# Performance work log

Hardware: AMD Instinct MI355X
Metric: run time of the kernel (lower is better)

## Reference

```python
import jax, jax.numpy as jnp
import numpy as np

N_NODES = 100000
N_EDGES = 1600000
F_IN = 128
N_HEADS = 4
F_OUT = 32
NEG_SLOPE = 0.2


def setup_inputs() -> dict:
    key = jax.random.key(0)
    k_feat, k_src, k_dst, k_w, k_as, k_ad, k_res = jax.random.split(key, 7)
    feat = jax.random.normal(k_feat, (N_NODES, F_IN), dtype=jnp.float32)
    src = jax.random.randint(k_src, (N_EDGES,), 0, N_NODES, dtype=jnp.int32)
    dst = jax.random.randint(k_dst, (N_EDGES,), 0, N_NODES, dtype=jnp.int32)
    s = 1.0 / np.sqrt(F_IN)
    W = jax.random.normal(k_w, (F_IN, N_HEADS * F_OUT), dtype=jnp.float32) * s
    att_src = jax.random.normal(k_as, (N_HEADS, F_OUT), dtype=jnp.float32) * 0.1
    att_dst = jax.random.normal(k_ad, (N_HEADS, F_OUT), dtype=jnp.float32) * 0.1
    W_res = jax.random.normal(k_res, (F_IN, N_HEADS * F_OUT), dtype=jnp.float32) * s
    return {"feat": feat, "W": W, "att_src": att_src, "att_dst": att_dst,
            "W_res": W_res, "src": src, "dst": dst}


def reference(feat, W, att_src, att_dst, W_res, src, dst):
    N = feat.shape[0]
    H, Fo = att_src.shape
    # shared linear projection (GATConv, bias=False): [N, H, Fo]
    x = (feat @ W).reshape(N, H, Fo)
    # per-node attention logits: [N, H]
    a_s = jnp.einsum('nhf,hf->nh', x, att_src)
    a_d = jnp.einsum('nhf,hf->nh', x, att_dst)
    # edge-wise scores + LeakyReLU: [E, H]
    e = jax.nn.leaky_relu(a_s[src] + a_d[dst], negative_slope=NEG_SLOPE)
    # segment softmax over incoming edges of each dst node
    e_max = jax.ops.segment_max(e, dst, num_segments=N)  # [N, H]
    e_exp = jnp.exp(e - e_max[dst])                       # [E, H]
    denom = jax.ops.segment_sum(e_exp, dst, num_segments=N)  # [N, H]
    alpha = e_exp / denom[dst]                            # [E, H]
    # weighted scatter-add aggregation: [N, H, Fo]
    msg = x[src] * alpha[:, :, None]
    out = jax.ops.segment_sum(msg, dst, num_segments=N)
    # residual projection
    res = (feat @ W_res).reshape(N, H, Fo)
    return out + res
```

## Files before the change

kernel.cpp:

```cpp
#include <hip/hip_runtime.h>
#include <math.h>

#define NN 100000
#define NE 1600000
#define F_IN 128
#define C 128
#define NEG_SLOPE 0.2f
#define PROJ_NB ((NN + 63) / 64)

#define NBLK1 256
#define EPB ((NE + NBLK1 - 1) / NBLK1)
#define BSHIFT 9
#define NBUCK ((NN + 511) / 512)

typedef __attribute__((ext_vector_type(8))) short short8;
typedef __attribute__((ext_vector_type(4))) float f32x4;
typedef __attribute__((ext_vector_type(4))) float floatx4;
typedef __attribute__((ext_vector_type(4))) unsigned short ushortx4;

static __device__ __forceinline__ unsigned short f2bf(float f) {
    unsigned int u = __float_as_uint(f);
    unsigned int r = (u + 0x7fff + ((u >> 16) & 1)) >> 16;
    return (unsigned short)r;
}
static __device__ __forceinline__ float bf2f(unsigned short h) {
    return __uint_as_float((unsigned int)h << 16);
}

__global__ __launch_bounds__(256)
void wconv_kernel(const float* __restrict__ W,
                  const float* __restrict__ Wr,
                  unsigned short* __restrict__ Btf)
{
    int g = blockIdx.x * 256 + threadIdx.x;
    int nt = g >> 8;
    int kc = (g >> 6) & 3;
    int l  = g & 63;
    int n  = nt * 16 + (l & 15);
    int kb = kc * 32 + (l >> 4) * 8;
    unsigned short v[8];
    #pragma unroll
    for (int j = 0; j < 8; ++j) {
        int k = kb + j;
        float f = (n < 128) ? W[(size_t)k * 128 + n] : Wr[(size_t)k * 128 + (n - 128)];
        v[j] = f2bf(f);
    }
    *(short8*)&Btf[(size_t)g * 8] = *(short8*)v;
}

__global__ __launch_bounds__(256, 4)
void proj_kernel(const float* __restrict__ feat,
                 const unsigned short* __restrict__ Btf,
                 const float* __restrict__ att_src,
                 const float* __restrict__ att_dst,
                 unsigned short* __restrict__ xb,
                 unsigned short* __restrict__ resb,
                 float* __restrict__ a_s,
                 float* __restrict__ a_d)
{
    __shared__ __align__(16) float T2all[4][16 * 68];
    __shared__ float s_as[64][4];
    __shared__ float s_ad[64][4];
    const int tid = threadIdx.x;

    const int base = blockIdx.x * 64;
    const int l = tid & 63;
    const int w = tid >> 6;
    const int quad = l >> 4;
    const int lo16 = l & 15;
    const int arow = w * 16 + lo16;
    const int nclamp = min(base + arow, NN - 1);

    short8 af[4];
    #pragma unroll
    for (int kc = 0; kc < 4; ++kc) {
        const float* fp = &feat[(size_t)nclamp * F_IN + kc * 32 + quad * 8];
        floatx4 f0 = __builtin_nontemporal_load((const floatx4*)fp);
        floatx4 f1 = __builtin_nontemporal_load((const floatx4*)(fp + 4));
        unsigned short v[8];
        v[0] = f2bf(f0.x); v[1] = f2bf(f0.y); v[2] = f2bf(f0.z); v[3] = f2bf(f0.w);
        v[4] = f2bf(f1.x); v[5] = f2bf(f1.y); v[6] = f2bf(f1.z); v[7] = f2bf(f1.w);
        af[kc] = *(short8*)v;
    }

    f32x4 acc[16];
    #pragma unroll
    for (int nt = 0; nt < 16; ++nt) acc[nt] = (f32x4){0.f, 0.f, 0.f, 0.f};

    #pragma unroll
    for (int nt = 0; nt < 16; ++nt) {
        const unsigned short* bp = &Btf[(size_t)(nt * 4) * 512 + l * 8];
        short8 b0 = *(const short8*)&bp[0];
        short8 b1 = *(const short8*)&bp[512];
        short8 b2 = *(const short8*)&bp[1024];
        short8 b3 = *(const short8*)&bp[1536];
        acc[nt] = __builtin_amdgcn_mfma_f32_16x16x32_bf16(af[0], b0, acc[nt], 0, 0, 0);
        acc[nt] = __builtin_amdgcn_mfma_f32_16x16x32_bf16(af[1], b1, acc[nt], 0, 0, 0);
        acc[nt] = __builtin_amdgcn_mfma_f32_16x16x32_bf16(af[2], b2, acc[nt], 0, 0, 0);
        acc[nt] = __builtin_amdgcn_mfma_f32_16x16x32_bf16(af[3], b3, acc[nt], 0, 0, 0);
    }

    float* T2 = T2all[w];
    const int g  = l >> 4;
    const int cf = (l & 15) * 4;

    #pragma unroll
    for (int p = 0; p < 2; ++p) {
        #pragma unroll
        for (int ntl = 0; ntl < 4; ++ntl) {
            int nt = p * 4 + ntl;
            #pragma unroll
            for (int r = 0; r < 4; ++r)
                T2[(quad * 4 + r) * 68 + ntl * 16 + lo16] = acc[nt][r];
        }
        floatx4 ws4 = *(const floatx4*)&att_src[p * 64 + cf];
        floatx4 wd4 = *(const floatx4*)&att_dst[p * 64 + cf];
        float ps[4], pd[4];
        #pragma unroll
        for (int it = 0; it < 4; ++it) {
            int row = it * 4 + g;
            floatx4 v = *(floatx4*)&T2[row * 68 + cf];
            int node = base + w * 16 + row;
            ushortx4 hh;
            hh.x = f2bf(v.x); hh.y = f2bf(v.y); hh.z = f2bf(v.z); hh.w = f2bf(v.w);
            if (node < NN)
                __builtin_nontemporal_store(hh,
                    (ushortx4*)&xb[(size_t)node * C + p * 64 + cf]);
            ps[it] = v.x * ws4.x + v.y * ws4.y + v.z * ws4.z + v.w * ws4.w;
            pd[it] = v.x * wd4.x + v.y * wd4.y + v.z * wd4.z + v.w * wd4.w;
        }
        #pragma unroll
        for (int it = 0; it < 4; ++it) {
            #pragma unroll
            for (int d = 1; d < 8; d <<= 1) {
                ps[it] += __shfl_xor(ps[it], d, 64);
                pd[it] += __shfl_xor(pd[it], d, 64);
            }
        }
        if ((l & 7) == 0) {
            int hh = p * 2 + ((l & 15) >> 3);
            #pragma unroll
            for (int it = 0; it < 4; ++it) {
                int lr = w * 16 + it * 4 + g;
                s_as[lr][hh] = ps[it];
                s_ad[lr][hh] = pd[it];
            }
        }
    }

    #pragma unroll
    for (int p = 0; p < 2; ++p) {
        #pragma unroll
        for (int ntl = 0; ntl < 4; ++ntl) {
            int nt = 8 + p * 4 + ntl;
            #pragma unroll
            for (int r = 0; r < 4; ++r)
                T2[(quad * 4 + r) * 68 + ntl * 16 + lo16] = acc[nt][r];
        }
        #pragma unroll
        for (int it = 0; it < 4; ++it) {
            int row = it * 4 + g;
            floatx4 v = *(floatx4*)&T2[row * 68 + cf];
            int node = base + w * 16 + row;
            ushortx4 hh;
            hh.x = f2bf(v.x); hh.y = f2bf(v.y); hh.z = f2bf(v.z); hh.w = f2bf(v.w);
            if (node < NN)
                __builtin_nontemporal_store(hh,
                    (ushortx4*)&resb[(size_t)node * C + p * 64 + cf]);
        }
    }

    __syncthreads();
    int idx = blockIdx.x * 256 + tid;
    if (idx < NN * 4) {
        a_s[idx] = ((float*)s_as)[tid];
        a_d[idx] = ((float*)s_ad)[tid];
    }
}

__global__ __launch_bounds__(256)
void sort1_kernel(const int* __restrict__ dst, int* __restrict__ counts)
{
    __shared__ int h[256];
    const int tid = threadIdx.x;
    h[tid] = 0;
    __syncthreads();
    const int e0 = blockIdx.x * EPB;
    const int e1 = min(NE, e0 + EPB);
    for (int e = e0 + tid; e < e1; e += 256)
        atomicAdd(&h[dst[e] >> BSHIFT], 1);
    __syncthreads();
    counts[blockIdx.x * 256 + tid] = h[tid];
}

__global__ __launch_bounds__(256)
void sortscan_kernel(int* __restrict__ counts, int* __restrict__ bucket_base)
{
    __shared__ int wsum[4];
    const int t = threadIdx.x, lane = t & 63, wid = t >> 6;
    int run = 0;
    #pragma unroll 8
    for (int b = 0; b < NBLK1; ++b) {
        int v = counts[b * 256 + t];
        counts[b * 256 + t] = run;
        run += v;
    }
    int v0 = run, v = run;
    #pragma unroll
    for (int off = 1; off < 64; off <<= 1) {
        int u = __shfl_up(v, off, 64);
        if (lane >= off) v += u;
    }
    if (lane == 63) wsum[wid] = v;
    __syncthreads();
    if (t == 0) {
        int r = 0;
        #pragma unroll
        for (int s = 0; s < 4; ++s) { int tmp = wsum[s]; wsum[s] = r; r += tmp; }
    }
    __syncthreads();
    int excl = wsum[wid] + (v - v0);
    bucket_base[t] = excl;
    if (t == 255) bucket_base[256] = excl + v0;
}

__global__ __launch_bounds__(256)
void sort2_kernel(const int* __restrict__ src, const int* __restrict__ dst,
                  const int* __restrict__ counts,
                  const int* __restrict__ bucket_base,
                  int* __restrict__ bpack)
{
    __shared__ int cur[256];
    const int tid = threadIdx.x;
    cur[tid] = bucket_base[tid] + counts[blockIdx.x * 256 + tid];
    __syncthreads();
    const int e0 = blockIdx.x * EPB;
    const int e1 = min(NE, e0 + EPB);
    for (int e = e0 + tid; e < e1; e += 256) {
        int d = dst[e];
        int s = src[e];
        int pos = atomicAdd(&cur[d >> BSHIFT], 1);
        bpack[pos] = ((d & 511) << 20) | s;
    }
}

__global__ __launch_bounds__(512)
void sort3_kernel(const int* __restrict__ bpack,
                  const int* __restrict__ bucket_base,
                  int* __restrict__ row_ptr,
                  int* __restrict__ csr_src)
{
    __shared__ int cnt[512];
    __shared__ int cur[512];
    __shared__ int wsum[8];
    const int t = threadIdx.x, lane = t & 63, wid = t >> 6;
    const int b = blockIdx.x;
    const int ebeg = bucket_base[b];
    const int eend = bucket_base[b + 1];
    cnt[t] = 0;
    __syncthreads();
    for (int e = ebeg + t; e < eend; e += 512)
        atomicAdd(&cnt[bpack[e] >> 20], 1);
    __syncthreads();
    int v0 = cnt[t], v = v0;
    #pragma unroll
    for (int off = 1; off < 64; off <<= 1) {
        int u = __shfl_up(v, off, 64);
        if (lane >= off) v += u;
    }
    if (lane == 63) wsum[wid] = v;
    __syncthreads();
    if (t == 0) {
        int r = 0;
        #pragma unroll
        for (int s = 0; s < 8; ++s) { int tmp = wsum[s]; wsum[s] = r; r += tmp; }
    }
    __syncthreads();
    int excl = wsum[wid] + (v - v0);
    cur[t] = excl;
    int n = (b << BSHIFT) + t;
    if (n < NN) row_ptr[n] = ebeg + excl;
    if (b == NBUCK - 1 && t == 0) row_ptr[NN] = NE;
    __syncthreads();
    for (int e = ebeg + t; e < eend; e += 512) {
        int p = bpack[e];
        int pos = atomicAdd(&cur[p >> 20], 1);
        csr_src[ebeg + pos] = p & 0xFFFFF;
    }
}

__global__ __launch_bounds__(256)
void agg_kernel(const unsigned short* __restrict__ xb,
                const unsigned short* __restrict__ resb,
                const float* __restrict__ a_s,
                const float* __restrict__ a_d,
                const int* __restrict__ row_ptr,
                const int* __restrict__ csr_src,
                float* __restrict__ out)
{
    __shared__ float s_alpha[4][4][68];
    __shared__ int   s_srcs[4][4][17];
    const int tid = threadIdx.x;
    const int w   = tid >> 6;
    const int l   = tid & 63;
    const int q   = l >> 4;
    const int t16 = l & 15;
    const int h   = t16 >> 2;

    const int n = blockIdx.x * 16 + w * 4 + q;
    const int r0  = row_ptr[n];
    const int deg = row_ptr[n + 1] - r0;

    short8 rv = *(const short8*)&resb[(size_t)n * C + t16 * 8];
    const float4 ad4 = *(const float4*)&a_d[n * 4];

    int dm = deg;
    dm = max(dm, __shfl_xor(dm, 16, 64));
    dm = max(dm, __shfl_xor(dm, 32, 64));

    float acc8[8];
    #pragma unroll
    for (int j = 0; j < 8; ++j) acc8[j] = 0.f;
    float dx = 0.f, dy = 0.f, dz = 0.f, dw = 0.f;

    for (int c0 = 0; c0 < dm; c0 += 16) {
        int e = c0 + t16;
        int s = 0;
        float4 ex = {0.f, 0.f, 0.f, 0.f};
        if (e < deg) {
            s = csr_src[r0 + e];
            float4 as4 = *(const float4*)&a_s[s * 4];
            float e0 = as4.x + ad4.x, e1 = as4.y + ad4.y;
            float e2 = as4.z + ad4.z, e3 = as4.w + ad4.w;
            e0 = (e0 > 0.f) ? e0 : NEG_SLOPE * e0;
            e1 = (e1 > 0.f) ? e1 : NEG_SLOPE * e1;
            e2 = (e2 > 0.f) ? e2 : NEG_SLOPE * e2;
            e3 = (e3 > 0.f) ? e3 : NEG_SLOPE * e3;
            ex.x = __expf(e0); ex.y = __expf(e1);
            ex.z = __expf(e2); ex.w = __expf(e3);
            dx += ex.x; dy += ex.y; dz += ex.z; dw += ex.w;
        }
        s_srcs[w][q][t16] = s;
        *(float4*)&s_alpha[w][q][t16 * 4] = ex;

        int cn = min(16, deg - c0);
        #pragma unroll 2
        for (int i = 0; i < cn; ++i) {
            int   si = s_srcs[w][q][i];
            float al = s_alpha[w][q][i * 4 + h];
            short8 uv = *(const short8*)&xb[(size_t)si * C + t16 * 8];
            acc8[0] = fmaf(al, bf2f((unsigned short)uv[0]), acc8[0]);
            acc8[1] = fmaf(al, bf2f((unsigned short)uv[1]), acc8[1]);
            acc8[2] = fmaf(al, bf2f((unsigned short)uv[2]), acc8[2]);
            acc8[3] = fmaf(al, bf2f((unsigned short)uv[3]), acc8[3]);
            acc8[4] = fmaf(al, bf2f((unsigned short)uv[4]), acc8[4]);
            acc8[5] = fmaf(al, bf2f((unsigned short)uv[5]), acc8[5]);
            acc8[6] = fmaf(al, bf2f((unsigned short)uv[6]), acc8[6]);
            acc8[7] = fmaf(al, bf2f((unsigned short)uv[7]), acc8[7]);
        }
    }

    #pragma unroll
    for (int d = 1; d < 16; d <<= 1) {
        dx += __shfl_xor(dx, d, 64);
        dy += __shfl_xor(dy, d, 64);
        dz += __shfl_xor(dz, d, 64);
        dw += __shfl_xor(dw, d, 64);
    }
    float den = (h == 0) ? dx : (h == 1) ? dy : (h == 2) ? dz : dw;
    float inv = (deg > 0) ? 1.f / den : 0.f;

    floatx4 o0, o1;
    o0.x = bf2f((unsigned short)rv[0]) + acc8[0] * inv;
    o0.y = bf2f((unsigned short)rv[1]) + acc8[1] * inv;
    o0.z = bf2f((unsigned short)rv[2]) + acc8[2] * inv;
    o0.w = bf2f((unsigned short)rv[3]) + acc8[3] * inv;
    o1.x = bf2f((unsigned short)rv[4]) + acc8[4] * inv;
    o1.y = bf2f((unsigned short)rv[5]) + acc8[5] * inv;
    o1.z = bf2f((unsigned short)rv[6]) + acc8[6] * inv;
    o1.w = bf2f((unsigned short)rv[7]) + acc8[7] * inv;
    __builtin_nontemporal_store(o0, (floatx4*)&out[(size_t)n * C + t16 * 8]);
    __builtin_nontemporal_store(o1, (floatx4*)&out[(size_t)n * C + t16 * 8 + 4]);
}

extern "C" void kernel_launch(void* const* d_in, const int* in_sizes, int n_in,
                              void* d_out, int out_size, void* d_ws, size_t ws_size,
                              hipStream_t stream)
{
    const float* feat    = (const float*)d_in[0];
    const float* W       = (const float*)d_in[1];
    const float* att_src = (const float*)d_in[2];
    const float* att_dst = (const float*)d_in[3];
    const float* W_res   = (const float*)d_in[4];
    const int*   src     = (const int*)d_in[5];
    const int*   dst     = (const int*)d_in[6];
    float* out = (float*)d_out;

    char* p = (char*)d_ws;
    unsigned short* xb   = (unsigned short*)p; p += (size_t)NN * C * sizeof(unsigned short);
    unsigned short* resb = (unsigned short*)p; p += (size_t)NN * C * sizeof(unsigned short);
    unsigned short* Btf  = (unsigned short*)p; p += (size_t)256 * 128 * sizeof(unsigned short);
    float* a_s = (float*)p;            p += (size_t)NN * 4 * sizeof(float);
    float* a_d = (float*)p;            p += (size_t)NN * 4 * sizeof(float);
    int* row_ptr = (int*)p;            p += (size_t)(NN + 1) * sizeof(int);
    int* counts  = (int*)p;            p += (size_t)NBLK1 * 256 * sizeof(int);
    int* bucket_base = (int*)p;        p += (size_t)257 * sizeof(int);
    int* bpack   = (int*)p;            p += (size_t)NE * sizeof(int);
    int* csr_src = (int*)p;            p += (size_t)NE * sizeof(int);

    wconv_kernel<<<16, 256, 0, stream>>>(W, W_res, Btf);
    proj_kernel<<<PROJ_NB, 256, 0, stream>>>(
        feat, Btf, att_src, att_dst, xb, resb, a_s, a_d);
    sort1_kernel<<<NBLK1, 256, 0, stream>>>(dst, counts);
    sortscan_kernel<<<1, 256, 0, stream>>>(counts, bucket_base);
    sort2_kernel<<<NBLK1, 256, 0, stream>>>(src, dst, counts, bucket_base, bpack);
    sort3_kernel<<<NBUCK, 512, 0, stream>>>(bpack, bucket_base, row_ptr, csr_src);
    agg_kernel<<<NN / 16, 256, 0, stream>>>(xb, resb, a_s, a_d, row_ptr, csr_src, out);
}
```

Measured before the change: 264.9 us.

## Edge-balanced aggregation with precomputed softmax denominators in sort pass

The softmax denominators are now computed in the bucket-sort kernel with LDS atomics and stored as inverse values, and the CSR keeps the packed local-dst bits. The aggregation kernel changes from one 16-lane group per node to 64 nodes per block, with each group taking an equal slice of the block's edges. Partial sums go into LDS accumulators through atomics whenever the destination changes, and the source gathers are software-pipelined two edges ahead. This targets load imbalance from varying degrees, at the cost of extra exp work and a_s/a_d gathers in sort3 plus LDS atomic traffic.

```diff
diff --git a/kernel.cpp b/kernel.cpp
--- a/kernel.cpp
+++ b/kernel.cpp
@@ -13,6 +13,10 @@
 #define BSHIFT 9
 #define NBUCK ((NN + 511) / 512)
 
+#define AGG_NB 64
+#define AGG_GRID ((NN + AGG_NB - 1) / AGG_NB)
+#define ASTRIDE 132
+
 typedef __attribute__((ext_vector_type(8))) short short8;
 typedef __attribute__((ext_vector_type(4))) float f32x4;
 typedef __attribute__((ext_vector_type(4))) float floatx4;
@@ -25,6 +29,9 @@
 }
 static __device__ __forceinline__ float bf2f(unsigned short h) {
     return __uint_as_float((unsigned int)h << 16);
+}
+static __device__ __forceinline__ float lrelu(float x) {
+    return (x > 0.f) ? x : NEG_SLOPE * x;
 }
 
 __global__ __launch_bounds__(256)
@@ -247,20 +254,36 @@
 __global__ __launch_bounds__(512)
 void sort3_kernel(const int* __restrict__ bpack,
                   const int* __restrict__ bucket_base,
+                  const float* __restrict__ a_s,
+                  const float* __restrict__ a_d,
                   int* __restrict__ row_ptr,
-                  int* __restrict__ csr_src)
+                  int* __restrict__ csr_pack,
+                  float* __restrict__ inv_den)
 {
     __shared__ int cnt[512];
-    __shared__ int cur[512];
+    __shared__ int curs[512];
     __shared__ int wsum[8];
+    __shared__ float sden[512 * 4];
     const int t = threadIdx.x, lane = t & 63, wid = t >> 6;
     const int b = blockIdx.x;
     const int ebeg = bucket_base[b];
     const int eend = bucket_base[b + 1];
     cnt[t] = 0;
-    __syncthreads();
-    for (int e = ebeg + t; e < eend; e += 512)
-        atomicAdd(&cnt[bpack[e] >> 20], 1);
+    #pragma unroll
+    for (int j = 0; j < 4; ++j) sden[t + j * 512] = 0.f;
+    __syncthreads();
+    for (int e = ebeg + t; e < eend; e += 512) {
+        int p = bpack[e];
+        int dl = p >> 20;
+        int s  = p & 0xFFFFF;
+        atomicAdd(&cnt[dl], 1);
+        float4 as4 = *(const float4*)&a_s[(size_t)s * 4];
+        float4 ad4 = *(const float4*)&a_d[(size_t)((b << BSHIFT) + dl) * 4];
+        atomicAdd(&sden[dl * 4 + 0], __expf(lrelu(as4.x + ad4.x)));
+        atomicAdd(&sden[dl * 4 + 1], __expf(lrelu(as4.y + ad4.y)));
+        atomicAdd(&sden[dl * 4 + 2], __expf(lrelu(as4.z + ad4.z)));
+        atomicAdd(&sden[dl * 4 + 3], __expf(lrelu(as4.w + ad4.w)));
+    }
     __syncthreads();
     int v0 = cnt[t], v = v0;
     #pragma unroll
@@ -277,15 +300,23 @@
     }
     __syncthreads();
     int excl = wsum[wid] + (v - v0);
-    cur[t] = excl;
+    curs[t] = excl;
     int n = (b << BSHIFT) + t;
-    if (n < NN) row_ptr[n] = ebeg + excl;
+    if (n < NN) {
+        row_ptr[n] = ebeg + excl;
+        float d0 = sden[t * 4 + 0], d1 = sden[t * 4 + 1];
+        float d2 = sden[t * 4 + 2], d3 = sden[t * 4 + 3];
+        inv_den[n * 4 + 0] = (d0 > 0.f) ? 1.f / d0 : 0.f;
+        inv_den[n * 4 + 1] = (d1 > 0.f) ? 1.f / d1 : 0.f;
+        inv_den[n * 4 + 2] = (d2 > 0.f) ? 1.f / d2 : 0.f;
+        inv_den[n * 4 + 3] = (d3 > 0.f) ? 1.f / d3 : 0.f;
+    }
     if (b == NBUCK - 1 && t == 0) row_ptr[NN] = NE;
     __syncthreads();
     for (int e = ebeg + t; e < eend; e += 512) {
         int p = bpack[e];
-        int pos = atomicAdd(&cur[p >> 20], 1);
-        csr_src[ebeg + pos] = p & 0xFFFFF;
+        int pos = atomicAdd(&curs[p >> 20], 1);
+        csr_pack[ebeg + pos] = p;
     }
 }
 
@@ -294,93 +325,122 @@
                 const unsigned short* __restrict__ resb,
                 const float* __restrict__ a_s,
                 const float* __restrict__ a_d,
+                const float* __restrict__ inv_den,
                 const int* __restrict__ row_ptr,
-                const int* __restrict__ csr_src,
+                const int* __restrict__ csr_pack,
                 float* __restrict__ out)
 {
-    __shared__ float s_alpha[4][4][68];
-    __shared__ int   s_srcs[4][4][17];
+    __shared__ float accL[AGG_NB * ASTRIDE];
+    __shared__ float lds_ad[AGG_NB * 4];
+    __shared__ float lds_inv[AGG_NB * 4];
     const int tid = threadIdx.x;
-    const int w   = tid >> 6;
-    const int l   = tid & 63;
-    const int q   = l >> 4;
-    const int t16 = l & 15;
+    const int n0 = blockIdx.x * AGG_NB;
+
+    {
+        int nidx = n0 * 4 + tid;
+        float adv = 0.f, ivv = 0.f;
+        if (nidx < NN * 4) { adv = a_d[nidx]; ivv = inv_den[nidx]; }
+        lds_ad[tid] = adv;
+        lds_inv[tid] = ivv;
+    }
+    #pragma unroll
+    for (int i = 0; i < (AGG_NB * ASTRIDE) / 256; ++i)
+        accL[tid + i * 256] = 0.f;
+
+    const int rp0 = row_ptr[n0];
+    const int rpN = row_ptr[min(n0 + AGG_NB, NN)];
+    __syncthreads();
+
+    const int ecnt = rpN - rp0;
+    const int gq  = tid >> 4;
+    const int t16 = tid & 15;
     const int h   = t16 >> 2;
-
-    const int n = blockIdx.x * 16 + w * 4 + q;
-    const int r0  = row_ptr[n];
-    const int deg = row_ptr[n + 1] - r0;
-
-    short8 rv = *(const short8*)&resb[(size_t)n * C + t16 * 8];
-    const float4 ad4 = *(const float4*)&a_d[n * 4];
-
-    int dm = deg;
-    dm = max(dm, __shfl_xor(dm, 16, 64));
-    dm = max(dm, __shfl_xor(dm, 32, 64));
-
-    float acc8[8];
-    #pragma unroll
-    for (int j = 0; j < 8; ++j) acc8[j] = 0.f;
-    float dx = 0.f, dy = 0.f, dz = 0.f, dw = 0.f;
-
-    for (int c0 = 0; c0 < dm; c0 += 16) {
-        int e = c0 + t16;
-        int s = 0;
-        float4 ex = {0.f, 0.f, 0.f, 0.f};
-        if (e < deg) {
-            s = csr_src[r0 + e];
-            float4 as4 = *(const float4*)&a_s[s * 4];
-            float e0 = as4.x + ad4.x, e1 = as4.y + ad4.y;
-            float e2 = as4.z + ad4.z, e3 = as4.w + ad4.w;
-            e0 = (e0 > 0.f) ? e0 : NEG_SLOPE * e0;
-            e1 = (e1 > 0.f) ? e1 : NEG_SLOPE * e1;
-            e2 = (e2 > 0.f) ? e2 : NEG_SLOPE * e2;
-            e3 = (e3 > 0.f) ? e3 : NEG_SLOPE * e3;
-            ex.x = __expf(e0); ex.y = __expf(e1);
-            ex.z = __expf(e2); ex.w = __expf(e3);
-            dx += ex.x; dy += ex.y; dz += ex.z; dw += ex.w;
-        }
-        s_srcs[w][q][t16] = s;
-        *(float4*)&s_alpha[w][q][t16 * 4] = ex;
-
-        int cn = min(16, deg - c0);
-        #pragma unroll 2
-        for (int i = 0; i < cn; ++i) {
-            int   si = s_srcs[w][q][i];
-            float al = s_alpha[w][q][i * 4 + h];
-            short8 uv = *(const short8*)&xb[(size_t)si * C + t16 * 8];
-            acc8[0] = fmaf(al, bf2f((unsigned short)uv[0]), acc8[0]);
-            acc8[1] = fmaf(al, bf2f((unsigned short)uv[1]), acc8[1]);
-            acc8[2] = fmaf(al, bf2f((unsigned short)uv[2]), acc8[2]);
-            acc8[3] = fmaf(al, bf2f((unsigned short)uv[3]), acc8[3]);
-            acc8[4] = fmaf(al, bf2f((unsigned short)uv[4]), acc8[4]);
-            acc8[5] = fmaf(al, bf2f((unsigned short)uv[5]), acc8[5]);
-            acc8[6] = fmaf(al, bf2f((unsigned short)uv[6]), acc8[6]);
-            acc8[7] = fmaf(al, bf2f((unsigned short)uv[7]), acc8[7]);
-        }
-    }
-
-    #pragma unroll
-    for (int d = 1; d < 16; d <<= 1) {
-        dx += __shfl_xor(dx, d, 64);
-        dy += __shfl_xor(dy, d, 64);
-        dz += __shfl_xor(dz, d, 64);
-        dw += __shfl_xor(dw, d, 64);
-    }
-    float den = (h == 0) ? dx : (h == 1) ? dy : (h == 2) ? dz : dw;
-    float inv = (deg > 0) ? 1.f / den : 0.f;
-
-    floatx4 o0, o1;
-    o0.x = bf2f((unsigned short)rv[0]) + acc8[0] * inv;
-    o0.y = bf2f((unsigned short)rv[1]) + acc8[1] * inv;
-    o0.z = bf2f((unsigned short)rv[2]) + acc8[2] * inv;
-    o0.w = bf2f((unsigned short)rv[3]) + acc8[3] * inv;
-    o1.x = bf2f((unsigned short)rv[4]) + acc8[4] * inv;
-    o1.y = bf2f((unsigned short)rv[5]) + acc8[5] * inv;
-    o1.z = bf2f((unsigned short)rv[6]) + acc8[6] * inv;
-    o1.w = bf2f((unsigned short)rv[7]) + acc8[7] * inv;
-    __builtin_nontemporal_store(o0, (floatx4*)&out[(size_t)n * C + t16 * 8]);
-    __builtin_nontemporal_store(o1, (floatx4*)&out[(size_t)n * C + t16 * 8 + 4]);
+    const int chunk = (ecnt + 15) >> 4;
+    const int ebeg = rp0 + gq * chunk;
+    const int eend = min(rpN, ebeg + chunk);
+
+    if (ebeg < eend) {
+        int p0 = csr_pack[ebeg];
+        int s0 = p0 & 0xFFFFF;
+        float as0 = a_s[(size_t)s0 * 4 + h];
+        short8 uv0 = *(const short8*)&xb[(size_t)s0 * C + t16 * 8];
+        int p1 = p0; float as1 = as0; short8 uv1 = uv0;
+        if (ebeg + 1 < eend) {
+            p1 = csr_pack[ebeg + 1];
+            int s1 = p1 & 0xFFFFF;
+            as1 = a_s[(size_t)s1 * 4 + h];
+            uv1 = *(const short8*)&xb[(size_t)s1 * C + t16 * 8];
+        }
+
+        int cur = (p0 >> 20) & 63;
+        float ad_h  = lds_ad[cur * 4 + h];
+        float inv_h = lds_inv[cur * 4 + h];
+        float a0 = 0.f, a1 = 0.f, a2 = 0.f, a3 = 0.f;
+        float a4 = 0.f, a5 = 0.f, a6 = 0.f, a7 = 0.f;
+
+        for (int e = ebeg; e < eend; ++e) {
+            int p2 = p0; float as2 = as0; short8 uv2 = uv0;
+            if (e + 2 < eend) {
+                p2 = csr_pack[e + 2];
+                int s2 = p2 & 0xFFFFF;
+                as2 = a_s[(size_t)s2 * 4 + h];
+                uv2 = *(const short8*)&xb[(size_t)s2 * C + t16 * 8];
+            }
+            int nl = (p0 >> 20) & 63;
+            if (nl != cur) {
+                float* fr = &accL[cur * ASTRIDE + t16 * 8];
+                atomicAdd(&fr[0], a0); atomicAdd(&fr[1], a1);
+                atomicAdd(&fr[2], a2); atomicAdd(&fr[3], a3);
+                atomicAdd(&fr[4], a4); atomicAdd(&fr[5], a5);
+                atomicAdd(&fr[6], a6); atomicAdd(&fr[7], a7);
+                a0 = a1 = a2 = a3 = a4 = a5 = a6 = a7 = 0.f;
+                cur = nl;
+                ad_h  = lds_ad[nl * 4 + h];
+                inv_h = lds_inv[nl * 4 + h];
+            }
+            float al = __expf(lrelu(as0 + ad_h)) * inv_h;
+            a0 = fmaf(al, bf2f((unsigned short)uv0[0]), a0);
+            a1 = fmaf(al, bf2f((unsigned short)uv0[1]), a1);
+            a2 = fmaf(al, bf2f((unsigned short)uv0[2]), a2);
+            a3 = fmaf(al, bf2f((unsigned short)uv0[3]), a3);
+            a4 = fmaf(al, bf2f((unsigned short)uv0[4]), a4);
+            a5 = fmaf(al, bf2f((unsigned short)uv0[5]), a5);
+            a6 = fmaf(al, bf2f((unsigned short)uv0[6]), a6);
+            a7 = fmaf(al, bf2f((unsigned short)uv0[7]), a7);
+            p0 = p1; as0 = as1; uv0 = uv1;
+            p1 = p2; as1 = as2; uv1 = uv2;
+        }
+        {
+            float* fr = &accL[cur * ASTRIDE + t16 * 8];
+            atomicAdd(&fr[0], a0); atomicAdd(&fr[1], a1);
+            atomicAdd(&fr[2], a2); atomicAdd(&fr[3], a3);
+            atomicAdd(&fr[4], a4); atomicAdd(&fr[5], a5);
+            atomicAdd(&fr[6], a6); atomicAdd(&fr[7], a7);
+        }
+    }
+    __syncthreads();
+
+    const int r  = tid >> 2;
+    const int c0 = (tid & 3) * 32;
+    const int n  = n0 + r;
+    if (n < NN) {
+        const float* ap = &accL[r * ASTRIDE + c0];
+        #pragma unroll
+        for (int j = 0; j < 32; j += 8) {
+            short8 rv = *(const short8*)&resb[(size_t)n * C + c0 + j];
+            floatx4 o0, o1;
+            o0.x = bf2f((unsigned short)rv[0]) + ap[j + 0];
+            o0.y = bf2f((unsigned short)rv[1]) + ap[j + 1];
+            o0.z = bf2f((unsigned short)rv[2]) + ap[j + 2];
+            o0.w = bf2f((unsigned short)rv[3]) + ap[j + 3];
+            o1.x = bf2f((unsigned short)rv[4]) + ap[j + 4];
+            o1.y = bf2f((unsigned short)rv[5]) + ap[j + 5];
+            o1.z = bf2f((unsigned short)rv[6]) + ap[j + 6];
+            o1.w = bf2f((unsigned short)rv[7]) + ap[j + 7];
+            __builtin_nontemporal_store(o0, (floatx4*)&out[(size_t)n * C + c0 + j]);
+            __builtin_nontemporal_store(o1, (floatx4*)&out[(size_t)n * C + c0 + j + 4]);
+        }
+    }
 }
 
 extern "C" void kernel_launch(void* const* d_in, const int* in_sizes, int n_in,
@@ -402,11 +462,12 @@
     unsigned short* Btf  = (unsigned short*)p; p += (size_t)256 * 128 * sizeof(unsigned short);
     float* a_s = (float*)p;            p += (size_t)NN * 4 * sizeof(float);
     float* a_d = (float*)p;            p += (size_t)NN * 4 * sizeof(float);
+    float* inv_den = (float*)p;        p += (size_t)NN * 4 * sizeof(float);
     int* row_ptr = (int*)p;            p += (size_t)(NN + 1) * sizeof(int);
     int* counts  = (int*)p;            p += (size_t)NBLK1 * 256 * sizeof(int);
     int* bucket_base = (int*)p;        p += (size_t)257 * sizeof(int);
     int* bpack   = (int*)p;            p += (size_t)NE * sizeof(int);
-    int* csr_src = (int*)p;            p += (size_t)NE * sizeof(int);
+    int* csr_pack = (int*)p;           p += (size_t)NE * sizeof(int);
 
     wconv_kernel<<<16, 256, 0, stream>>>(W, W_res, Btf);
     proj_kernel<<<PROJ_NB, 256, 0, stream>>>(
@@ -414,6 +475,8 @@
     sort1_kernel<<<NBLK1, 256, 0, stream>>>(dst, counts);
     sortscan_kernel<<<1, 256, 0, stream>>>(counts, bucket_base);
     sort2_kernel<<<NBLK1, 256, 0, stream>>>(src, dst, counts, bucket_base, bpack);
-    sort3_kernel<<<NBUCK, 512, 0, stream>>>(bpack, bucket_base, row_ptr, csr_src);
-    agg_kernel<<<NN / 16, 256, 0, stream>>>(xb, resb, a_s, a_d, row_ptr, csr_src, out);
-}
+    sort3_kernel<<<NBUCK, 512, 0, stream>>>(bpack, bucket_base, a_s, a_d,
+                                            row_ptr, csr_pack, inv_den);
+    agg_kernel<<<AGG_GRID, 256, 0, stream>>>(xb, resb, a_s, a_d, inv_den,
+                                             row_ptr, csr_pack, out);
+}
```

New measurement: 372.0 us. 1.4x slower.

## Merge independent sort and projection kernels into heterogeneous fused launches

Applied to the files above, without the earlier changes.

Combines weight conversion with the dst histogram in one launch, and the bucket scatter with the MFMA projection in another, using block-index dispatch so independent work runs concurrently. This cuts the launch count from seven to five and lets the small sort phases overlap the projection. The counts array is transposed to a bucket-major layout so the single-block scan can read it with int4 vector loads. The trade-off is that shared memory is sized for the larger role and the proj-role occupancy bound now also applies to the scatter blocks.

```diff
diff --git a/kernel.cpp b/kernel.cpp
--- a/kernel.cpp
+++ b/kernel.cpp
@@ -13,6 +13,10 @@
 #define BSHIFT 9
 #define NBUCK ((NN + 511) / 512)
 
+#define WCONV_NB 16
+#define FAT1_NB (WCONV_NB + NBLK1)
+#define FAT2_NB (NBLK1 + PROJ_NB)
+
 typedef __attribute__((ext_vector_type(8))) short short8;
 typedef __attribute__((ext_vector_type(4))) float f32x4;
 typedef __attribute__((ext_vector_type(4))) float floatx4;
@@ -26,30 +30,93 @@
 static __device__ __forceinline__ float bf2f(unsigned short h) {
     return __uint_as_float((unsigned int)h << 16);
 }
+static __device__ __forceinline__ float lrelu(float x) {
+    return (x > 0.f) ? x : NEG_SLOPE * x;
+}
 
 __global__ __launch_bounds__(256)
-void wconv_kernel(const float* __restrict__ W,
-                  const float* __restrict__ Wr,
-                  unsigned short* __restrict__ Btf)
-{
-    int g = blockIdx.x * 256 + threadIdx.x;
-    int nt = g >> 8;
-    int kc = (g >> 6) & 3;
-    int l  = g & 63;
-    int n  = nt * 16 + (l & 15);
-    int kb = kc * 32 + (l >> 4) * 8;
-    unsigned short v[8];
-    #pragma unroll
-    for (int j = 0; j < 8; ++j) {
-        int k = kb + j;
-        float f = (n < 128) ? W[(size_t)k * 128 + n] : Wr[(size_t)k * 128 + (n - 128)];
-        v[j] = f2bf(f);
-    }
-    *(short8*)&Btf[(size_t)g * 8] = *(short8*)v;
+void fat1_kernel(const float* __restrict__ W,
+                 const float* __restrict__ Wr,
+                 unsigned short* __restrict__ Btf,
+                 const int* __restrict__ dst,
+                 int* __restrict__ counts)
+{
+    __shared__ int h[256];
+    const int tid = threadIdx.x;
+
+    if (blockIdx.x < WCONV_NB) {
+        int g = blockIdx.x * 256 + tid;
+        int nt = g >> 8;
+        int kc = (g >> 6) & 3;
+        int l  = g & 63;
+        int n  = nt * 16 + (l & 15);
+        int kb = kc * 32 + (l >> 4) * 8;
+        unsigned short v[8];
+        #pragma unroll
+        for (int j = 0; j < 8; ++j) {
+            int k = kb + j;
+            float f = (n < 128) ? W[(size_t)k * 128 + n]
+                                : Wr[(size_t)k * 128 + (n - 128)];
+            v[j] = f2bf(f);
+        }
+        *(short8*)&Btf[(size_t)g * 8] = *(short8*)v;
+        return;
+    }
+
+    const int hb = blockIdx.x - WCONV_NB;
+    h[tid] = 0;
+    __syncthreads();
+    const int e0 = hb * EPB;
+    const int e1 = min(NE, e0 + EPB);
+    for (int e = e0 + tid; e < e1; e += 256)
+        atomicAdd(&h[dst[e] >> BSHIFT], 1);
+    __syncthreads();
+    counts[tid * NBLK1 + hb] = h[tid];
+}
+
+__global__ __launch_bounds__(256)
+void sortscan_kernel(int* __restrict__ counts, int* __restrict__ bucket_base)
+{
+    __shared__ int wsum[4];
+    const int t = threadIdx.x, lane = t & 63, wid = t >> 6;
+    const int base = t * NBLK1;
+    int run = 0;
+    #pragma unroll 8
+    for (int g = 0; g < NBLK1 / 4; ++g) {
+        int4 c = *(const int4*)&counts[base + g * 4];
+        int4 w;
+        w.x = run;
+        w.y = w.x + c.x;
+        w.z = w.y + c.y;
+        w.w = w.z + c.z;
+        run = w.w + c.w;
+        *(int4*)&counts[base + g * 4] = w;
+    }
+    int v0 = run, v = run;
+    #pragma unroll
+    for (int off = 1; off < 64; off <<= 1) {
+        int u = __shfl_up(v, off, 64);
+        if (lane >= off) v += u;
+    }
+    if (lane == 63) wsum[wid] = v;
+    __syncthreads();
+    if (t == 0) {
+        int r = 0;
+        #pragma unroll
+        for (int s = 0; s < 4; ++s) { int tmp = wsum[s]; wsum[s] = r; r += tmp; }
+    }
+    __syncthreads();
+    int excl = wsum[wid] + (v - v0);
+    bucket_base[t] = excl;
+    if (t == 255) bucket_base[256] = excl + v0;
 }
 
 __global__ __launch_bounds__(256, 4)
-void proj_kernel(const float* __restrict__ feat,
+void fat2_kernel(const int* __restrict__ src, const int* __restrict__ dst,
+                 const int* __restrict__ counts,
+                 const int* __restrict__ bucket_base,
+                 int* __restrict__ bpack,
+                 const float* __restrict__ feat,
                  const unsigned short* __restrict__ Btf,
                  const float* __restrict__ att_src,
                  const float* __restrict__ att_dst,
@@ -58,12 +125,30 @@
                  float* __restrict__ a_s,
                  float* __restrict__ a_d)
 {
-    __shared__ __align__(16) float T2all[4][16 * 68];
-    __shared__ float s_as[64][4];
-    __shared__ float s_ad[64][4];
+    __shared__ __align__(16) char smem[19456];
     const int tid = threadIdx.x;
 
-    const int base = blockIdx.x * 64;
+    if (blockIdx.x < NBLK1) {
+        int* cur = (int*)smem;
+        cur[tid] = bucket_base[tid] + counts[tid * NBLK1 + blockIdx.x];
+        __syncthreads();
+        const int e0 = blockIdx.x * EPB;
+        const int e1 = min(NE, e0 + EPB);
+        for (int e = e0 + tid; e < e1; e += 256) {
+            int d = dst[e];
+            int s = src[e];
+            int pos = atomicAdd(&cur[d >> BSHIFT], 1);
+            bpack[pos] = ((d & 511) << 20) | s;
+        }
+        return;
+    }
+
+    const int pb = blockIdx.x - NBLK1;
+    float* T2base = (float*)smem;
+    float (*s_as)[4] = (float(*)[4])(smem + 17408);
+    float (*s_ad)[4] = (float(*)[4])(smem + 18432);
+
+    const int base = pb * 64;
     const int l = tid & 63;
     const int w = tid >> 6;
     const int quad = l >> 4;
@@ -100,7 +185,7 @@
         acc[nt] = __builtin_amdgcn_mfma_f32_16x16x32_bf16(af[3], b3, acc[nt], 0, 0, 0);
     }
 
-    float* T2 = T2all[w];
+    float* T2 = T2base + w * (16 * 68);
     const int g  = l >> 4;
     const int cf = (l & 15) * 4;
 
@@ -171,76 +256,10 @@
     }
 
     __syncthreads();
-    int idx = blockIdx.x * 256 + tid;
+    int idx = pb * 256 + tid;
     if (idx < NN * 4) {
         a_s[idx] = ((float*)s_as)[tid];
         a_d[idx] = ((float*)s_ad)[tid];
-    }
-}
-
-__global__ __launch_bounds__(256)
-void sort1_kernel(const int* __restrict__ dst, int* __restrict__ counts)
-{
-    __shared__ int h[256];
-    const int tid = threadIdx.x;
-    h[tid] = 0;
-    __syncthreads();
-    const int e0 = blockIdx.x * EPB;
-    const int e1 = min(NE, e0 + EPB);
-    for (int e = e0 + tid; e < e1; e += 256)
-        atomicAdd(&h[dst[e] >> BSHIFT], 1);
-    __syncthreads();
-    counts[blockIdx.x * 256 + tid] = h[tid];
-}
-
-__global__ __launch_bounds__(256)
-void sortscan_kernel(int* __restrict__ counts, int* __restrict__ bucket_base)
-{
-    __shared__ int wsum[4];
-    const int t = threadIdx.x, lane = t & 63, wid = t >> 6;
-    int run = 0;
-    #pragma unroll 8
-    for (int b = 0; b < NBLK1; ++b) {
-        int v = counts[b * 256 + t];
-        counts[b * 256 + t] = run;
-        run += v;
-    }
-    int v0 = run, v = run;
-    #pragma unroll
-    for (int off = 1; off < 64; off <<= 1) {
-        int u = __shfl_up(v, off, 64);
-        if (lane >= off) v += u;
-    }
-    if (lane == 63) wsum[wid] = v;
-    __syncthreads();
-    if (t == 0) {
-        int r = 0;
-        #pragma unroll
-        for (int s = 0; s < 4; ++s) { int tmp = wsum[s]; wsum[s] = r; r += tmp; }
-    }
-    __syncthreads();
-    int excl = wsum[wid] + (v - v0);
-    bucket_base[t] = excl;
-    if (t == 255) bucket_base[256] = excl + v0;
-}
-
-__global__ __launch_bounds__(256)
-void sort2_kernel(const int* __restrict__ src, const int* __restrict__ dst,
-                  const int* __restrict__ counts,
-                  const int* __restrict__ bucket_base,
-                  int* __restrict__ bpack)
-{
-    __shared__ int cur[256];
-    const int tid = threadIdx.x;
-    cur[tid] = bucket_base[tid] + counts[blockIdx.x * 256 + tid];
-    __syncthreads();
-    const int e0 = blockIdx.x * EPB;
-    const int e1 = min(NE, e0 + EPB);
-    for (int e = e0 + tid; e < e1; e += 256) {
-        int d = dst[e];
-        int s = src[e];
-        int pos = atomicAdd(&cur[d >> BSHIFT], 1);
-        bpack[pos] = ((d & 511) << 20) | s;
     }
 }
 
@@ -330,14 +349,10 @@
         if (e < deg) {
             s = csr_src[r0 + e];
             float4 as4 = *(const float4*)&a_s[s * 4];
-            float e0 = as4.x + ad4.x, e1 = as4.y + ad4.y;
-            float e2 = as4.z + ad4.z, e3 = as4.w + ad4.w;
-            e0 = (e0 > 0.f) ? e0 : NEG_SLOPE * e0;
-            e1 = (e1 > 0.f) ? e1 : NEG_SLOPE * e1;
-            e2 = (e2 > 0.f) ? e2 : NEG_SLOPE * e2;
-            e3 = (e3 > 0.f) ? e3 : NEG_SLOPE * e3;
-            ex.x = __expf(e0); ex.y = __expf(e1);
-            ex.z = __expf(e2); ex.w = __expf(e3);
+            ex.x = __expf(lrelu(as4.x + ad4.x));
+            ex.y = __expf(lrelu(as4.y + ad4.y));
+            ex.z = __expf(lrelu(as4.z + ad4.z));
+            ex.w = __expf(lrelu(as4.w + ad4.w));
             dx += ex.x; dy += ex.y; dz += ex.z; dw += ex.w;
         }
         s_srcs[w][q][t16] = s;
@@ -408,12 +423,11 @@
     int* bpack   = (int*)p;            p += (size_t)NE * sizeof(int);
     int* csr_src = (int*)p;            p += (size_t)NE * sizeof(int);
 
-    wconv_kernel<<<16, 256, 0, stream>>>(W, W_res, Btf);
-    proj_kernel<<<PROJ_NB, 256, 0, stream>>>(
-        feat, Btf, att_src, att_dst, xb, resb, a_s, a_d);
-    sort1_kernel<<<NBLK1, 256, 0, stream>>>(dst, counts);
+    fat1_kernel<<<FAT1_NB, 256, 0, stream>>>(W, W_res, Btf, dst, counts);
     sortscan_kernel<<<1, 256, 0, stream>>>(counts, bucket_base);
-    sort2_kernel<<<NBLK1, 256, 0, stream>>>(src, dst, counts, bucket_base, bpack);
+    fat2_kernel<<<FAT2_NB, 256, 0, stream>>>(src, dst, counts, bucket_base, bpack,
+                                             feat, Btf, att_src, att_dst,
+                                             xb, resb, a_s, a_d);
     sort3_kernel<<<NBUCK, 512, 0, stream>>>(bpack, bucket_base, row_ptr, csr_src);
     agg_kernel<<<NN / 16, 256, 0, stream>>>(xb, resb, a_s, a_d, row_ptr, csr_src, out);
 }
```

Measured after the change: 262.9 us. About the same (-0.8%).
